# Kernel tuning notes

Measured on AMD Instinct MI355X. Metric: run time of the kernel, lower is better.

Reference implementation:

```python
import jax, jax.numpy as jnp
import numpy as np

VIS_ENC_DIM = 1024
SENT_HIDDEN_DIM = 512
ATT_DIM = 512
B, L = 64, 1024


def setup_inputs() -> dict:
    key = jax.random.key(0)
    ks = jax.random.split(key, 8)
    s_enc = 1.0 / np.sqrt(VIS_ENC_DIM)
    s_dec = 1.0 / np.sqrt(SENT_HIDDEN_DIM)
    s_full = 1.0 / np.sqrt(ATT_DIM)
    return {
        "vis_enc_output": jax.random.normal(ks[0], (B, L, VIS_ENC_DIM), jnp.float32),
        "dec_hidden_state": jax.random.normal(ks[1], (B, SENT_HIDDEN_DIM), jnp.float32),
        "W_enc": jax.random.uniform(ks[2], (VIS_ENC_DIM, ATT_DIM), jnp.float32, -s_enc, s_enc),
        "b_enc": jax.random.uniform(ks[3], (ATT_DIM,), jnp.float32, -s_enc, s_enc),
        "W_dec": jax.random.uniform(ks[4], (SENT_HIDDEN_DIM, ATT_DIM), jnp.float32, -s_dec, s_dec),
        "b_dec": jax.random.uniform(ks[5], (ATT_DIM,), jnp.float32, -s_dec, s_dec),
        "w_full": jax.random.uniform(ks[6], (ATT_DIM,), jnp.float32, -s_full, s_full),
        "b_full": jax.random.uniform(ks[7], (), jnp.float32, -s_full, s_full),
    }


def reference(vis_enc_output, dec_hidden_state, W_enc, b_enc, W_dec, b_dec, w_full, b_full):
    # enc projection: [B, L, A]
    vis_enc_att = jnp.einsum('blv,va->bla', vis_enc_output, W_enc) + b_enc
    # dec projection: [B, A]
    dec_output = dec_hidden_state @ W_dec + b_dec
    # broadcast add + tanh, then reduce over att dim -> scores [B, L]
    joined = jnp.tanh(vis_enc_att + dec_output[:, None, :])
    logits = jnp.einsum('bla,a->bl', joined, w_full) + b_full
    att_scores = jax.nn.softmax(logits, axis=1)
    # weighted sum over L -> [B, V]
    att_output = jnp.einsum('bl,blv->bv', att_scores, vis_enc_output)
    return att_output, att_scores
```

## Files before the change

### kernel.cpp

```cpp
#include <hip/hip_runtime.h>
#include <hip/hip_bf16.h>
#include <stdint.h>


typedef __attribute__((ext_vector_type(8))) short bf16x8;
typedef __attribute__((ext_vector_type(8))) unsigned short ushortx8;
typedef __attribute__((ext_vector_type(4))) float f32x4;

#define LOG2E 1.4426950408889634f

__device__ __forceinline__ unsigned short f2bf(float f) {
  uint32_t u = __builtin_bit_cast(uint32_t, f);
  u += 0x7FFFu + ((u >> 16) & 1u);
  return (unsigned short)(u >> 16);
}

__device__ __forceinline__ float fast_tanh(float x) {
  float e = __builtin_amdgcn_exp2f(x * 2.885390081777927f);
  return 1.0f - 2.0f * __builtin_amdgcn_rcpf(e + 1.0f);
}

__device__ __forceinline__ void load_lds16(const void* g, void* l) {
  __builtin_amdgcn_global_load_lds(
      (const __attribute__((address_space(1))) void*)g,
      (__attribute__((address_space(3))) void*)l, 16, 0, 0);
}

__global__ __launch_bounds__(256) void k01_prep(const float* __restrict__ W,
                                                unsigned short* __restrict__ Wst,
                                                const float* __restrict__ dec,
                                                const float* __restrict__ Wd,
                                                const float* __restrict__ bd,
                                                const float* __restrict__ be,
                                                float* __restrict__ dproj,
                                                float* __restrict__ out) {
  const int tid = threadIdx.x;
  if (blockIdx.x < 256) {
    const int S = blockIdx.x * 256 + tid;
    const int t = S >> 11;
    const int kb = (S >> 9) & 3;
    const int a = S & 511;
    const int k0 = t * 32 + kb * 8;
    ushortx8 p;
#pragma unroll
    for (int j = 0; j < 8; ++j) p[j] = f2bf(W[(size_t)(k0 + j) * 512 + a]);
    *(ushortx8*)(Wst + (size_t)S * 8) = p;
  } else {
    const int q = blockIdx.x - 256;
    out[q * 256 + tid] = 0.0f;
    const int b = q >> 2;
    const int a = (q & 3) * 128 + (tid & 127);
    const int hh = tid >> 7;
    const float* dr = dec + b * 512 + hh * 256;
    const float* wc = Wd + (size_t)(hh * 256) * 512 + a;
    float acc = 0.f;
#pragma unroll 8
    for (int h = 0; h < 256; ++h) acc = fmaf(dr[h], wc[(size_t)h * 512], acc);
    __shared__ float sh[128];
    if (hh == 1) sh[tid & 127] = acc;
    __syncthreads();
    if (hh == 0) dproj[b * 512 + a] = acc + sh[tid] + bd[a] + be[a];
  }
}

__global__ __launch_bounds__(512, 1) void k2_fused_gemm(
    const float* __restrict__ vis, const unsigned short* __restrict__ Wst,
    const float* __restrict__ dproj, const float* __restrict__ wfull,
    float* __restrict__ logits) {
  alignas(16) __shared__ unsigned short Al[2][4096];
  alignas(16) __shared__ unsigned short Bl[2][16384];

  const int tid = threadIdx.x;
  const int lane = tid & 63;
  const int w = tid >> 6;
  const int wm = w >> 2;
  const int wn = w & 3;
  const int blk = blockIdx.x;
  const int b = blk >> 3;
  const size_t mbase = (size_t)blk * 128;

  const int arow = tid >> 2;
  const int akb = tid & 3;
  const float* asrc = vis + (mbase + (size_t)arow) * 1024 + akb * 8;
  const int a_dst = akb * 1024 + arow * 8;

  const unsigned short* bsrc = Wst + (size_t)w * 2048 + (size_t)lane * 8;

  f32x4 acc[4][8];
#pragma unroll
  for (int m = 0; m < 4; ++m)
#pragma unroll
    for (int n = 0; n < 8; ++n) acc[m][n] = (f32x4){0.f, 0.f, 0.f, 0.f};

  const int a_rd = (lane >> 4) * 1024 + (wm * 64 + (lane & 15)) * 8;
  const int b_rd = (lane >> 4) * 4096 + (wn * 128 + (lane & 15)) * 8;

  f32x4 xA0, xA1;
  xA0 = *(const f32x4*)(asrc);
  xA1 = *(const f32x4*)(asrc + 4);
#pragma unroll
  for (int j = 0; j < 4; ++j)
    load_lds16(bsrc + j * 512, &Bl[0][w * 2048 + j * 512]);
  {
    ushortx8 p;
    p[0] = f2bf(xA0[0]); p[1] = f2bf(xA0[1]); p[2] = f2bf(xA0[2]); p[3] = f2bf(xA0[3]);
    p[4] = f2bf(xA1[0]); p[5] = f2bf(xA1[1]); p[6] = f2bf(xA1[2]); p[7] = f2bf(xA1[3]);
    *(ushortx8*)(&Al[0][a_dst]) = p;
  }

  for (int t = 0; t < 32; ++t) {
    const int cur = t & 1;
    __syncthreads();
    if (t < 31) {
      const float* as = asrc + (size_t)(t + 1) * 32;
      xA0 = *(const f32x4*)(as);
      xA1 = *(const f32x4*)(as + 4);
      const unsigned short* bs = bsrc + (size_t)(t + 1) * 16384;
#pragma unroll
      for (int j = 0; j < 4; ++j)
        load_lds16(bs + j * 512, &Bl[cur ^ 1][w * 2048 + j * 512]);
    }
    bf16x8 af[4];
#pragma unroll
    for (int m = 0; m < 4; ++m) af[m] = *(const bf16x8*)(&Al[cur][a_rd + m * 128]);
    bf16x8 bfr[8];
#pragma unroll
    for (int n = 0; n < 8; ++n) bfr[n] = *(const bf16x8*)(&Bl[cur][b_rd + n * 128]);
#pragma unroll
    for (int m = 0; m < 4; ++m)
#pragma unroll
      for (int n = 0; n < 8; ++n)
        acc[m][n] = __builtin_amdgcn_mfma_f32_16x16x32_bf16(af[m], bfr[n], acc[m][n], 0, 0, 0);
    if (t < 31) {
      ushortx8 p;
      p[0] = f2bf(xA0[0]); p[1] = f2bf(xA0[1]); p[2] = f2bf(xA0[2]); p[3] = f2bf(xA0[3]);
      p[4] = f2bf(xA1[0]); p[5] = f2bf(xA1[1]); p[6] = f2bf(xA1[2]); p[7] = f2bf(xA1[3]);
      *(ushortx8*)(&Al[cur ^ 1][a_dst]) = p;
    }
  }

  const float* dp = dproj + b * 512 + wn * 128 + (lane & 15);
  const float* wf = wfull + wn * 128 + (lane & 15);
  float dpv[8], wfv[8];
#pragma unroll
  for (int n = 0; n < 8; ++n) { dpv[n] = dp[n * 16]; wfv[n] = wf[n * 16]; }

  float* Lred = (float*)Al;
  __syncthreads();

#pragma unroll
  for (int m = 0; m < 4; ++m) {
#pragma unroll
    for (int r = 0; r < 4; ++r) {
      float s = 0.f;
#pragma unroll
      for (int n = 0; n < 8; ++n)
        s += wfv[n] * fast_tanh(acc[m][n][r] + dpv[n]);
      s += __shfl_xor(s, 1, 64);
      s += __shfl_xor(s, 2, 64);
      s += __shfl_xor(s, 4, 64);
      s += __shfl_xor(s, 8, 64);
      if ((lane & 15) == 0) {
        int row = wm * 64 + m * 16 + (lane >> 4) * 4 + r;
        Lred[row * 4 + wn] = s;
      }
    }
  }
  __syncthreads();
  if (tid < 128) {
    f32x4 v = *(const f32x4*)(&Lred[tid * 4]);
    logits[mbase + tid] = v[0] + v[1] + v[2] + v[3];
  }
}

__global__ __launch_bounds__(256) void k34_attout(const float* __restrict__ logits,
                                                  const float* __restrict__ vis,
                                                  float* __restrict__ out) {
  const int b = blockIdx.x;
  const int chunk = blockIdx.y;
  const int tid = threadIdx.x;
  const int wid = tid >> 6;
  const int lane = tid & 63;
  const float* base = logits + b * 1024;

  float x[4];
#pragma unroll
  for (int j = 0; j < 4; ++j) x[j] = base[j * 256 + tid];
  float mx = fmaxf(fmaxf(x[0], x[1]), fmaxf(x[2], x[3]));
#pragma unroll
  for (int d = 1; d < 64; d <<= 1) mx = fmaxf(mx, __shfl_xor(mx, d, 64));
  __shared__ float redm[4], reds[4];
  if (lane == 0) redm[wid] = mx;
  __syncthreads();
  mx = fmaxf(fmaxf(redm[0], redm[1]), fmaxf(redm[2], redm[3]));
  float s = 0.f;
#pragma unroll
  for (int j = 0; j < 4; ++j) s += __builtin_amdgcn_exp2f((x[j] - mx) * LOG2E);
#pragma unroll
  for (int d = 1; d < 64; d <<= 1) s += __shfl_xor(s, d, 64);
  if (lane == 0) reds[wid] = s;
  __syncthreads();
  s = reds[0] + reds[1] + reds[2] + reds[3];
  const float inv = 1.0f / s;

  if (chunk == 0) {
#pragma unroll
    for (int j = 0; j < 4; ++j)
      out[65536 + b * 1024 + j * 256 + tid] =
          __builtin_amdgcn_exp2f((x[j] - mx) * LOG2E) * inv;
  }

  __shared__ float p[128];
  const int l0 = chunk * 128;
  if (tid < 128)
    p[tid] = __builtin_amdgcn_exp2f((base[l0 + tid] - mx) * LOG2E) * inv;
  __syncthreads();

  const f32x4* vb = (const f32x4*)(vis + ((size_t)b * 1024 + (size_t)l0) * 1024) + tid;
  f32x4 acc0 = (f32x4){0.f, 0.f, 0.f, 0.f};
  f32x4 acc1 = (f32x4){0.f, 0.f, 0.f, 0.f};
#pragma unroll 4
  for (int l = 0; l < 128; l += 2) {
    acc0 += vb[(size_t)l * 256] * p[l];
    acc1 += vb[(size_t)(l + 1) * 256] * p[l + 1];
  }
  f32x4 acc = acc0 + acc1;
  float* o = out + b * 1024 + tid * 4;
  atomicAdd(o + 0, acc[0]);
  atomicAdd(o + 1, acc[1]);
  atomicAdd(o + 2, acc[2]);
  atomicAdd(o + 3, acc[3]);
}

extern "C" void kernel_launch(void* const* d_in, const int* in_sizes, int n_in,
                              void* d_out, int out_size, void* d_ws, size_t ws_size,
                              hipStream_t stream) {
  const float* vis = (const float*)d_in[0];
  const float* dec = (const float*)d_in[1];
  const float* Wenc = (const float*)d_in[2];
  const float* benc = (const float*)d_in[3];
  const float* Wdec = (const float*)d_in[4];
  const float* bdec = (const float*)d_in[5];
  const float* wfull = (const float*)d_in[6];
  float* out = (float*)d_out;
  char* ws = (char*)d_ws;
  unsigned short* Wst = (unsigned short*)ws;
  float* dproj = (float*)(ws + (1 << 20));
  float* logits = (float*)(ws + (1 << 20) + (128 << 10));

  hipLaunchKernelGGL(k01_prep, dim3(512), dim3(256), 0, stream,
                     Wenc, Wst, dec, Wdec, bdec, benc, dproj, out);
  hipLaunchKernelGGL(k2_fused_gemm, dim3(512), dim3(512), 0, stream,
                     vis, Wst, dproj, wfull, logits);
  hipLaunchKernelGGL(k34_attout, dim3(64, 8), dim3(256), 0, stream,
                     logits, vis, out);
}
```

Baseline: 509.5 us.

## Pre-convert vis to tiled bf16 and shrink GEMM tiles with register-held B

Adds a prep pass that converts the fp32 vis tensor to bf16 in a pre-tiled layout. The GEMM can then stage A with direct global-to-LDS loads and read W fragments straight from global into registers, dropping the LDS copy of B. The GEMM block shrinks to 64 rows and 256 threads, with two blocks per CU and a two-stage unrolled loop. This removes the in-loop fp32 conversion and cuts LDS use, but adds a full extra pass over vis (read 256MB fp32, write 128MB bf16), which may cost more than it saves.

Result: slower. 531.3 us (+4.3%).

```diff
diff --git a/kernel.cpp b/kernel.cpp
--- a/kernel.cpp
+++ b/kernel.cpp
@@ -5,6 +5,7 @@
 
 typedef __attribute__((ext_vector_type(8))) short bf16x8;
 typedef __attribute__((ext_vector_type(8))) unsigned short ushortx8;
+typedef __attribute__((ext_vector_type(4))) unsigned short ushortx4;
 typedef __attribute__((ext_vector_type(4))) float f32x4;
 
 #define LOG2E 1.4426950408889634f
@@ -26,7 +27,9 @@
       (__attribute__((address_space(3))) void*)l, 16, 0, 0);
 }
 
-__global__ __launch_bounds__(256) void k01_prep(const float* __restrict__ W,
+__global__ __launch_bounds__(256) void k01_prep(const float* __restrict__ vis,
+                                                unsigned short* __restrict__ visb,
+                                                const float* __restrict__ W,
                                                 unsigned short* __restrict__ Wst,
                                                 const float* __restrict__ dec,
                                                 const float* __restrict__ Wd,
@@ -34,19 +37,44 @@
                                                 const float* __restrict__ be,
                                                 float* __restrict__ dproj,
                                                 float* __restrict__ out) {
+  __shared__ unsigned short S[16 * 1040];
   const int tid = threadIdx.x;
-  if (blockIdx.x < 256) {
-    const int S = blockIdx.x * 256 + tid;
-    const int t = S >> 11;
-    const int kb = (S >> 9) & 3;
-    const int a = S & 511;
+
+  if (blockIdx.x < 4096) {
+    const int c = blockIdx.x;
+    const size_t vbase = (size_t)c * 16 * 1024;
+#pragma unroll
+    for (int p = 0; p < 16; ++p) {
+      f32x4 x = *(const f32x4*)(vis + vbase + p * 1024 + tid * 4);
+      ushortx4 u;
+      u[0] = f2bf(x[0]); u[1] = f2bf(x[1]); u[2] = f2bf(x[2]); u[3] = f2bf(x[3]);
+      *(ushortx4*)(&S[p * 1040 + tid * 4]) = u;
+    }
+    __syncthreads();
+    const int blk = c >> 2;
+    const int rb = (c & 3) * 16;
+    const int s = tid >> 1;
+    const int h = tid & 1;
+    const int t = s >> 2;
+    const int kb = s & 3;
+    unsigned short* dst =
+        visb + (((size_t)blk * 32 + t) * 256 + kb * 64 + rb + h * 8) * 8;
+    const unsigned short* srcS = &S[(h * 8) * 1040 + t * 32 + kb * 8];
+#pragma unroll
+    for (int r = 0; r < 8; ++r)
+      *(ushortx8*)(dst + r * 8) = *(const ushortx8*)(srcS + r * 1040);
+  } else if (blockIdx.x < 4352) {
+    const int Sl = (blockIdx.x - 4096) * 256 + tid;
+    const int t = Sl >> 11;
+    const int kb = (Sl >> 9) & 3;
+    const int a = Sl & 511;
     const int k0 = t * 32 + kb * 8;
     ushortx8 p;
 #pragma unroll
     for (int j = 0; j < 8; ++j) p[j] = f2bf(W[(size_t)(k0 + j) * 512 + a]);
-    *(ushortx8*)(Wst + (size_t)S * 8) = p;
+    *(ushortx8*)(Wst + (size_t)Sl * 8) = p;
   } else {
-    const int q = blockIdx.x - 256;
+    const int q = blockIdx.x - 4352;
     out[q * 256 + tid] = 0.0f;
     const int b = q >> 2;
     const int a = (q & 3) * 128 + (tid & 127);
@@ -56,35 +84,29 @@
     float acc = 0.f;
 #pragma unroll 8
     for (int h = 0; h < 256; ++h) acc = fmaf(dr[h], wc[(size_t)h * 512], acc);
-    __shared__ float sh[128];
+    float* sh = (float*)S;
     if (hh == 1) sh[tid & 127] = acc;
     __syncthreads();
     if (hh == 0) dproj[b * 512 + a] = acc + sh[tid] + bd[a] + be[a];
   }
 }
 
-__global__ __launch_bounds__(512, 1) void k2_fused_gemm(
-    const float* __restrict__ vis, const unsigned short* __restrict__ Wst,
+__global__ __launch_bounds__(256, 2) void k2_fused_gemm(
+    const unsigned short* __restrict__ visb, const unsigned short* __restrict__ Wst,
     const float* __restrict__ dproj, const float* __restrict__ wfull,
     float* __restrict__ logits) {
-  alignas(16) __shared__ unsigned short Al[2][4096];
-  alignas(16) __shared__ unsigned short Bl[2][16384];
+  alignas(16) __shared__ unsigned short Al[2][2048];
 
   const int tid = threadIdx.x;
   const int lane = tid & 63;
-  const int w = tid >> 6;
-  const int wm = w >> 2;
-  const int wn = w & 3;
+  const int wn = tid >> 6;
   const int blk = blockIdx.x;
-  const int b = blk >> 3;
-  const size_t mbase = (size_t)blk * 128;
-
-  const int arow = tid >> 2;
-  const int akb = tid & 3;
-  const float* asrc = vis + (mbase + (size_t)arow) * 1024 + akb * 8;
-  const int a_dst = akb * 1024 + arow * 8;
-
-  const unsigned short* bsrc = Wst + (size_t)w * 2048 + (size_t)lane * 8;
+  const int b = blk >> 4;
+  const size_t mbase = (size_t)blk * 64;
+
+  const unsigned short* agsrc = visb + ((size_t)blk * 32 * 256 + tid) * 8;
+  const ushortx8* bbase = (const ushortx8*)Wst +
+                          ((size_t)(lane >> 4) * 512 + wn * 128 + (lane & 15));
 
   f32x4 acc[4][8];
 #pragma unroll
@@ -92,52 +114,41 @@
 #pragma unroll
     for (int n = 0; n < 8; ++n) acc[m][n] = (f32x4){0.f, 0.f, 0.f, 0.f};
 
-  const int a_rd = (lane >> 4) * 1024 + (wm * 64 + (lane & 15)) * 8;
-  const int b_rd = (lane >> 4) * 4096 + (wn * 128 + (lane & 15)) * 8;
-
-  f32x4 xA0, xA1;
-  xA0 = *(const f32x4*)(asrc);
-  xA1 = *(const f32x4*)(asrc + 4);
-#pragma unroll
-  for (int j = 0; j < 4; ++j)
-    load_lds16(bsrc + j * 512, &Bl[0][w * 2048 + j * 512]);
-  {
-    ushortx8 p;
-    p[0] = f2bf(xA0[0]); p[1] = f2bf(xA0[1]); p[2] = f2bf(xA0[2]); p[3] = f2bf(xA0[3]);
-    p[4] = f2bf(xA1[0]); p[5] = f2bf(xA1[1]); p[6] = f2bf(xA1[2]); p[7] = f2bf(xA1[3]);
-    *(ushortx8*)(&Al[0][a_dst]) = p;
-  }
-
-  for (int t = 0; t < 32; ++t) {
-    const int cur = t & 1;
-    __syncthreads();
-    if (t < 31) {
-      const float* as = asrc + (size_t)(t + 1) * 32;
-      xA0 = *(const f32x4*)(as);
-      xA1 = *(const f32x4*)(as + 4);
-      const unsigned short* bs = bsrc + (size_t)(t + 1) * 16384;
-#pragma unroll
-      for (int j = 0; j < 4; ++j)
-        load_lds16(bs + j * 512, &Bl[cur ^ 1][w * 2048 + j * 512]);
-    }
-    bf16x8 af[4];
-#pragma unroll
-    for (int m = 0; m < 4; ++m) af[m] = *(const bf16x8*)(&Al[cur][a_rd + m * 128]);
-    bf16x8 bfr[8];
-#pragma unroll
-    for (int n = 0; n < 8; ++n) bfr[n] = *(const bf16x8*)(&Bl[cur][b_rd + n * 128]);
-#pragma unroll
-    for (int m = 0; m < 4; ++m)
-#pragma unroll
-      for (int n = 0; n < 8; ++n)
-        acc[m][n] = __builtin_amdgcn_mfma_f32_16x16x32_bf16(af[m], bfr[n], acc[m][n], 0, 0, 0);
-    if (t < 31) {
-      ushortx8 p;
-      p[0] = f2bf(xA0[0]); p[1] = f2bf(xA0[1]); p[2] = f2bf(xA0[2]); p[3] = f2bf(xA0[3]);
-      p[4] = f2bf(xA1[0]); p[5] = f2bf(xA1[1]); p[6] = f2bf(xA1[2]); p[7] = f2bf(xA1[3]);
-      *(ushortx8*)(&Al[cur ^ 1][a_dst]) = p;
-    }
-  }
+  const int a_rd = (lane >> 4) * 512 + (lane & 15) * 8;
+
+#define STAGEA(t, buf) load_lds16(agsrc + (size_t)(t) * 2048, &Al[buf][wn * 512])
+#define LOADB(t, arr)                                                    \
+  {                                                                      \
+    const ushortx8* bp = bbase + (size_t)(t) * 2048;                     \
+    _Pragma("unroll") for (int n = 0; n < 8; ++n)                        \
+        arr[n] = *(const bf16x8*)(bp + n * 16);                          \
+  }
+#define COMPUTE(buf, arr)                                                \
+  {                                                                      \
+    bf16x8 af[4];                                                        \
+    _Pragma("unroll") for (int m = 0; m < 4; ++m)                        \
+        af[m] = *(const bf16x8*)(&Al[buf][a_rd + m * 128]);              \
+    _Pragma("unroll") for (int m = 0; m < 4; ++m)                        \
+        _Pragma("unroll") for (int n = 0; n < 8; ++n)                    \
+            acc[m][n] = __builtin_amdgcn_mfma_f32_16x16x32_bf16(         \
+                af[m], arr[n], acc[m][n], 0, 0, 0);                      \
+  }
+
+  bf16x8 bA[8], bB[8];
+  STAGEA(0, 0);
+  LOADB(0, bA);
+
+  for (int tt = 0; tt < 32; tt += 2) {
+    __syncthreads();
+    if (tt < 31) { STAGEA(tt + 1, 1); LOADB(tt + 1, bB); }
+    COMPUTE(0, bA);
+    __syncthreads();
+    if (tt + 1 < 31) { STAGEA(tt + 2, 0); LOADB(tt + 2, bA); }
+    COMPUTE(1, bB);
+  }
+#undef STAGEA
+#undef LOADB
+#undef COMPUTE
 
   const float* dp = dproj + b * 512 + wn * 128 + (lane & 15);
   const float* wf = wfull + wn * 128 + (lane & 15);
@@ -161,13 +172,13 @@
       s += __shfl_xor(s, 4, 64);
       s += __shfl_xor(s, 8, 64);
       if ((lane & 15) == 0) {
-        int row = wm * 64 + m * 16 + (lane >> 4) * 4 + r;
+        int row = m * 16 + (lane >> 4) * 4 + r;
         Lred[row * 4 + wn] = s;
       }
     }
   }
   __syncthreads();
-  if (tid < 128) {
+  if (tid < 64) {
     f32x4 v = *(const f32x4*)(&Lred[tid * 4]);
     logits[mbase + tid] = v[0] + v[1] + v[2] + v[3];
   }
@@ -247,11 +258,12 @@
   unsigned short* Wst = (unsigned short*)ws;
   float* dproj = (float*)(ws + (1 << 20));
   float* logits = (float*)(ws + (1 << 20) + (128 << 10));
-
-  hipLaunchKernelGGL(k01_prep, dim3(512), dim3(256), 0, stream,
-                     Wenc, Wst, dec, Wdec, bdec, benc, dproj, out);
-  hipLaunchKernelGGL(k2_fused_gemm, dim3(512), dim3(512), 0, stream,
-                     vis, Wst, dproj, wfull, logits);
+  unsigned short* visb = (unsigned short*)(ws + (2 << 20));
+
+  hipLaunchKernelGGL(k01_prep, dim3(4608), dim3(256), 0, stream,
+                     vis, visb, Wenc, Wst, dec, Wdec, bdec, benc, dproj, out);
+  hipLaunchKernelGGL(k2_fused_gemm, dim3(1024), dim3(256), 0, stream,
+                     visb, Wst, dproj, wfull, logits);
   hipLaunchKernelGGL(k34_attout, dim3(64, 8), dim3(256), 0, stream,
                      logits, vis, out);
 }
```
